# Performance work log

Measured on AMD Instinct MI355X. Metric: run time of the kernel, lower is better.

## Reference

```python
import jax, jax.numpy as jnp
import numpy as np

D_MODEL = 64  # per-head dim; temper = sqrt(D_MODEL)
NEG_INF = -1e30  # stand-in for -inf; safe under softmax and autodiff


def setup_inputs() -> dict:
    key = jax.random.key(0)
    kq, kk, kv, km = jax.random.split(key, 4)
    B, S, D = 16, 2048, 64
    q = jax.random.normal(kq, (B, S, D), dtype=jnp.float32)
    k = jax.random.normal(kk, (B, S, D), dtype=jnp.float32)
    v = jax.random.normal(kv, (B, S, D), dtype=jnp.float32)
    attn_mask = jax.random.bernoulli(km, 0.1, (B, S, S))
    return {"q": q, "k": k, "v": v, "attn_mask": attn_mask}


def reference(q, k, v, attn_mask):
    temper = jnp.sqrt(jnp.float32(D_MODEL))
    # [B, Sq, Sk] scores
    attn = jnp.einsum("bqd,bkd->bqk", q, k) / temper
    attn = jnp.where(attn_mask, NEG_INF, attn)
    attn = jax.nn.softmax(attn, axis=2)
    # dropout is identity in eval / attn_dropout=0.0
    output = jnp.einsum("bqk,bkd->bqd", attn, v)
    return (output, attn)
```

## Files before the change

kernel.cpp:

```cpp
#include <hip/hip_runtime.h>
#include <hip/hip_bf16.h>
#include <stdint.h>


#define S_DIM 2048
#define D_DIM 64

typedef short short8 __attribute__((ext_vector_type(8)));
typedef float floatx4 __attribute__((ext_vector_type(4)));
typedef unsigned short ushort8v __attribute__((ext_vector_type(8)));
typedef uint32_t u32a __attribute__((may_alias));

__device__ __forceinline__ unsigned short f2bf(float x) {
    uint32_t u = __float_as_uint(x);
    u += 0x7fffu + ((u >> 16) & 1u);
    return (unsigned short)(u >> 16);
}
__device__ __forceinline__ float bf2f(unsigned short h) {
    return __uint_as_float((uint32_t)h << 16);
}

__global__ __launch_bounds__(256) void prep_all(
    const int* __restrict__ mask, uint32_t* __restrict__ bits,
    const float* __restrict__ k,
    unsigned short* __restrict__ khi2, unsigned short* __restrict__ klo2,
    const float* __restrict__ v, unsigned short* __restrict__ vfrag)
{
    const int blk = blockIdx.x;
    const int tid = threadIdx.x;

    if (blk < 8192) {
        const size_t base = (size_t)blk * 8192;
        const int lane = tid & 63;
        const size_t wbase = base + (size_t)(tid & ~63);
        #pragma unroll
        for (int j = 0; j < 32; ++j) {
            int m = mask[base + j * 256 + tid];
            unsigned long long bal = __ballot(m != 0);
            if ((lane & 31) == 0) {
                size_t wb = wbase + j * 256;
                bits[(wb >> 5) + (lane >> 5)] = (uint32_t)(bal >> ((lane >> 5) * 32));
            }
        }
    } else if (blk < 9216) {
        const int e  = blk - 8192;
        const int b  = e >> 6;
        const int kc = (e & 63) * 2 + (tid >> 7);
        const int t  = tid & 127;
        const int s = t >> 6, quad = (t >> 4) & 3, n16 = t & 15;
        const float* src = k + ((size_t)(b * S_DIM) + kc * 16 + n16) * D_DIM + s * 32 + quad * 8;
        float4 x0 = *(const float4*)src;
        float4 x1 = *(const float4*)(src + 4);
        float xs[8] = {x0.x, x0.y, x0.z, x0.w, x1.x, x1.y, x1.z, x1.w};
        ushort8v h, l;
        #pragma unroll
        for (int p = 0; p < 8; ++p) {
            unsigned short hp = f2bf(xs[p]);
            h[p] = hp;
            l[p] = f2bf(xs[p] - bf2f(hp));
        }
        size_t o = ((size_t)(b * 128 + kc)) * 1024 + (size_t)t * 8;
        *(ushort8v*)(khi2 + o) = h;
        *(ushort8v*)(klo2 + o) = l;
    } else {
        const int e  = blk - 9216;
        const int b  = e >> 6;
        const int kb = e & 63;
        const int nc = tid >> 6, quad = (tid >> 4) & 3, n16 = tid & 15;
        ushort8v o;
        #pragma unroll
        for (int p = 0; p < 8; ++p) {
            float x = v[((size_t)(b * S_DIM) + kb * 32 + quad * 8 + p) * D_DIM + nc * 16 + n16];
            o[p] = f2bf(x);
        }
        *(ushort8v*)(vfrag + ((size_t)(b * 64 + kb)) * 2048 + (size_t)tid * 8) = o;
    }
}

__global__ __launch_bounds__(512) void attn_fused_v4(
    const float* __restrict__ q,
    const unsigned short* __restrict__ khi2, const unsigned short* __restrict__ klo2,
    const unsigned short* __restrict__ vfrag,
    const uint32_t* __restrict__ bits,
    float* __restrict__ out, float* __restrict__ attn)
{
    __shared__ __align__(16) float qlds[16 * 68];
    __shared__ __align__(16) unsigned short pbuf[8 * 16 * 36];
    __shared__ __align__(16) float obuf[8 * 16 * 68];
    __shared__ float mxtab[8 * 16];
    __shared__ float ltab[8 * 16];

    const int tid  = threadIdx.x;
    const int w    = tid >> 6;
    const int lane = tid & 63;
    const int quad = lane >> 4;
    const int n16  = lane & 15;
    const int b    = blockIdx.x >> 7;
    const int q0   = (blockIdx.x & 127) * 16;
    const int key0 = w * 256;

    uint32_t blo, bhi;
    {
        const uint32_t* bsrc = bits +
            ((size_t)(b * S_DIM) + q0 + (lane >> 2)) * 64 + w * 8 + 2 * (lane & 3);
        uint2 bt = *(const uint2*)bsrc;
        blo = bt.x; bhi = bt.y;
    }

    {
        int m = tid >> 5, d = (tid & 31) * 2;
        float2 qv = *(const float2*)(q + ((size_t)(b * S_DIM + q0 + m)) * D_DIM + d);
        qlds[m * 68 + d]     = qv.x;
        qlds[m * 68 + d + 1] = qv.y;
    }
    __syncthreads();

    short8 ahi[2], alo[2];
    #pragma unroll
    for (int s = 0; s < 2; ++s) {
        const float* qp = &qlds[n16 * 68 + s * 32 + quad * 8];
        union { unsigned short u[8]; short8 v; } H, L;
        #pragma unroll
        for (int p = 0; p < 8; ++p) {
            float x = qp[p];
            unsigned short hp = f2bf(x);
            H.u[p] = hp;
            L.u[p] = f2bf(x - bf2f(hp));
        }
        ahi[s] = H.v; alo[s] = L.v;
    }

    floatx4 sc[16];
    const unsigned short* khb = khi2 + (size_t)b * 131072;
    const unsigned short* klb = klo2 + (size_t)b * 131072;
    #pragma unroll
    for (int c = 0; c < 16; ++c) {
        const int kc = w * 16 + c;
        floatx4 acc = {0.f, 0.f, 0.f, 0.f};
        #pragma unroll
        for (int s = 0; s < 2; ++s) {
            const size_t off = (size_t)((kc * 2 + s) * 4 + quad) * 128 + n16 * 8;
            short8 BH = *(const short8*)(khb + off);
            short8 BL = *(const short8*)(klb + off);
            acc = __builtin_amdgcn_mfma_f32_16x16x32_bf16(ahi[s], BH, acc, 0, 0, 0);
            acc = __builtin_amdgcn_mfma_f32_16x16x32_bf16(ahi[s], BL, acc, 0, 0, 0);
            acc = __builtin_amdgcn_mfma_f32_16x16x32_bf16(alo[s], BH, acc, 0, 0, 0);
        }
        sc[c] = acc;
    }
    #pragma unroll
    for (int r = 0; r < 4; ++r) {
        #pragma unroll
        for (int c = 0; c < 16; ++c) {
            int srcl = quad * 16 + r * 4 + (c >> 2);
            uint32_t d = (uint32_t)__shfl((int)((c & 2) ? bhi : blo), srcl, 64);
            uint32_t bit = (d >> ((c & 1) * 16 + n16)) & 1u;
            sc[c][r] = bit ? -1e30f : sc[c][r] * 0.125f;
        }
    }

    #pragma unroll
    for (int r = 0; r < 4; ++r) {
        float mx = sc[0][r];
        #pragma unroll
        for (int c = 1; c < 16; ++c) mx = fmaxf(mx, sc[c][r]);
        #pragma unroll
        for (int o = 1; o < 16; o <<= 1) mx = fmaxf(mx, __shfl_xor(mx, o, 64));
        if (n16 == 0) mxtab[w * 16 + quad * 4 + r] = mx;
    }
    __syncthreads();
    #pragma unroll
    for (int r = 0; r < 4; ++r) {
        float mf = -3e38f;
        #pragma unroll
        for (int w2 = 0; w2 < 8; ++w2) mf = fmaxf(mf, mxtab[w2 * 16 + quad * 4 + r]);
        float l = 0.f;
        #pragma unroll
        for (int c = 0; c < 16; ++c) {
            float e = __expf(sc[c][r] - mf);
            sc[c][r] = e;
            l += e;
        }
        #pragma unroll
        for (int o = 1; o < 16; o <<= 1) l += __shfl_xor(l, o, 64);
        if (n16 == 0) ltab[w * 16 + quad * 4 + r] = l;
    }
    __syncthreads();
    #pragma unroll
    for (int r = 0; r < 4; ++r) {
        float l = 0.f;
        #pragma unroll
        for (int w2 = 0; w2 < 8; ++w2) l += ltab[w2 * 16 + quad * 4 + r];
        float inv = 1.0f / l;
        #pragma unroll
        for (int c = 0; c < 16; ++c) sc[c][r] *= inv;
    }

    {
        float* arow = attn + (size_t)(b * S_DIM + q0 + quad * 4) * S_DIM + key0 + n16;
        #pragma unroll
        for (int c = 0; c < 16; ++c) {
            #pragma unroll
            for (int r = 0; r < 4; ++r)
                __builtin_nontemporal_store(sc[c][r], arow + (size_t)r * S_DIM + c * 16);
        }
    }

    floatx4 o0 = {0,0,0,0}, o1 = {0,0,0,0}, o2 = {0,0,0,0}, o3 = {0,0,0,0};
    unsigned short* pw = pbuf + w * 576;
    const unsigned short* vtb = vfrag + (size_t)b * 131072;
    #pragma unroll
    for (int s2 = 0; s2 < 8; ++s2) {
        #pragma unroll
        for (int h = 0; h < 2; ++h) {
            const int c = s2 * 2 + h;
            #pragma unroll
            for (int r = 0; r < 4; ++r)
                pw[(quad * 4 + r) * 36 + h * 16 + n16] = f2bf(sc[c][r]);
        }
        short8 pa;
        {
            const u32a* pr = (const u32a*)((const char*)pbuf +
                                   (size_t)w * 1152 + n16 * 72 + quad * 16);
            union { uint32_t u[4]; short8 v; } P;
            P.u[0] = pr[0]; P.u[1] = pr[1]; P.u[2] = pr[2]; P.u[3] = pr[3];
            pa = P.v;
        }
        const int kb = w * 8 + s2;
        #pragma unroll
        for (int nc = 0; nc < 4; ++nc) {
            const size_t off = (size_t)((kb * 4 + nc) * 4 + quad) * 128 + n16 * 8;
            short8 bv = *(const short8*)(vtb + off);
            floatx4& oo = (nc == 0 ? o0 : nc == 1 ? o1 : nc == 2 ? o2 : o3);
            oo = __builtin_amdgcn_mfma_f32_16x16x32_bf16(pa, bv, oo, 0, 0, 0);
        }
    }

    #pragma unroll
    for (int nc = 0; nc < 4; ++nc) {
        floatx4 oo = (nc == 0 ? o0 : nc == 1 ? o1 : nc == 2 ? o2 : o3);
        #pragma unroll
        for (int i = 0; i < 4; ++i)
            obuf[(w * 16 + quad * 4 + i) * 68 + nc * 16 + n16] = oo[i];
    }
    __syncthreads();
    #pragma unroll
    for (int t2 = 0; t2 < 2; ++t2) {
        int idx = tid + t2 * 512;
        int m = idx >> 6, d = idx & 63;
        float a = 0.f;
        #pragma unroll
        for (int w2 = 0; w2 < 8; ++w2) a += obuf[(w2 * 16 + m) * 68 + d];
        out[(size_t)(b * S_DIM + q0 + m) * D_DIM + d] = a;
    }
}

__global__ __launch_bounds__(512) void attn_fused_v1(
    const float* __restrict__ q, const float* __restrict__ k,
    const float* __restrict__ v, const int* __restrict__ mask,
    float* __restrict__ out, float* __restrict__ attn)
{
    __shared__ __align__(16) float qlds[16 * 68];
    __shared__ __align__(16) unsigned short pbuf[8 * 16 * 36];
    __shared__ __align__(16) float obuf[8 * 16 * 68];
    __shared__ float mxtab[8 * 16];
    __shared__ float ltab[8 * 16];

    const int tid  = threadIdx.x;
    const int w    = tid >> 6;
    const int lane = tid & 63;
    const int quad = lane >> 4;
    const int n16  = lane & 15;
    const int b    = blockIdx.x >> 7;
    const int q0   = (blockIdx.x & 127) * 16;
    const int key0 = w * 256;

    {
        int m = tid >> 5, d = (tid & 31) * 2;
        float2 qv = *(const float2*)(q + ((size_t)(b * S_DIM + q0 + m)) * D_DIM + d);
        qlds[m * 68 + d]     = qv.x;
        qlds[m * 68 + d + 1] = qv.y;
    }
    __syncthreads();

    short8 ahi[2], alo[2];
    #pragma unroll
    for (int s = 0; s < 2; ++s) {
        const float* qp = &qlds[n16 * 68 + s * 32 + quad * 8];
        union { __hip_bfloat162 h[4]; short8 v; } H, L;
        #pragma unroll
        for (int p = 0; p < 4; ++p) {
            float x0 = qp[2 * p], x1 = qp[2 * p + 1];
            __hip_bfloat162 h2 = __float22bfloat162_rn(float2{x0, x1});
            float l0 = x0 - __bfloat162float(h2.x);
            float l1 = x1 - __bfloat162float(h2.y);
            H.h[p] = h2;
            L.h[p] = __float22bfloat162_rn(float2{l0, l1});
        }
        ahi[s] = H.v; alo[s] = L.v;
    }

    floatx4 sc[16];
    const size_t kvbase = (size_t)(b * S_DIM) * D_DIM;
    #pragma unroll
    for (int c = 0; c < 16; ++c) {
        const int key = key0 + c * 16 + n16;
        const int* mp = mask + (size_t)(b * S_DIM + q0 + quad * 4) * S_DIM + key;
        int mk0 = mp[0], mk1 = mp[S_DIM], mk2 = mp[2 * S_DIM], mk3 = mp[3 * S_DIM];
        floatx4 acc = {0.f, 0.f, 0.f, 0.f};
        #pragma unroll
        for (int s = 0; s < 2; ++s) {
            const float* kp = k + kvbase + (size_t)key * D_DIM + s * 32 + quad * 8;
            float4 k0 = *(const float4*)kp;
            float4 k1 = *(const float4*)(kp + 4);
            float kf[8] = {k0.x, k0.y, k0.z, k0.w, k1.x, k1.y, k1.z, k1.w};
            union { __hip_bfloat162 h[4]; short8 v; } BH, BL;
            #pragma unroll
            for (int p = 0; p < 4; ++p) {
                float x0 = kf[2 * p], x1 = kf[2 * p + 1];
                __hip_bfloat162 h2 = __float22bfloat162_rn(float2{x0, x1});
                BH.h[p] = h2;
                BL.h[p] = __float22bfloat162_rn(
                    float2{x0 - __bfloat162float(h2.x), x1 - __bfloat162float(h2.y)});
            }
            acc = __builtin_amdgcn_mfma_f32_16x16x32_bf16(ahi[s], BH.v, acc, 0, 0, 0);
            acc = __builtin_amdgcn_mfma_f32_16x16x32_bf16(ahi[s], BL.v, acc, 0, 0, 0);
            acc = __builtin_amdgcn_mfma_f32_16x16x32_bf16(alo[s], BH.v, acc, 0, 0, 0);
        }
        sc[c][0] = mk0 ? -1e30f : acc[0] * 0.125f;
        sc[c][1] = mk1 ? -1e30f : acc[1] * 0.125f;
        sc[c][2] = mk2 ? -1e30f : acc[2] * 0.125f;
        sc[c][3] = mk3 ? -1e30f : acc[3] * 0.125f;
    }

    #pragma unroll
    for (int r = 0; r < 4; ++r) {
        float mx = sc[0][r];
        #pragma unroll
        for (int c = 1; c < 16; ++c) mx = fmaxf(mx, sc[c][r]);
        #pragma unroll
        for (int o = 1; o < 16; o <<= 1) mx = fmaxf(mx, __shfl_xor(mx, o, 64));
        if (n16 == 0) mxtab[w * 16 + quad * 4 + r] = mx;
    }
    __syncthreads();
    #pragma unroll
    for (int r = 0; r < 4; ++r) {
        float mf = -3e38f;
        #pragma unroll
        for (int w2 = 0; w2 < 8; ++w2) mf = fmaxf(mf, mxtab[w2 * 16 + quad * 4 + r]);
        float l = 0.f;
        #pragma unroll
        for (int c = 0; c < 16; ++c) {
            float e = __expf(sc[c][r] - mf);
            sc[c][r] = e;
            l += e;
        }
        #pragma unroll
        for (int o = 1; o < 16; o <<= 1) l += __shfl_xor(l, o, 64);
        if (n16 == 0) ltab[w * 16 + quad * 4 + r] = l;
    }
    __syncthreads();
    #pragma unroll
    for (int r = 0; r < 4; ++r) {
        float l = 0.f;
        #pragma unroll
        for (int w2 = 0; w2 < 8; ++w2) l += ltab[w2 * 16 + quad * 4 + r];
        float inv = 1.0f / l;
        #pragma unroll
        for (int c = 0; c < 16; ++c) sc[c][r] *= inv;
    }

    {
        float* arow = attn + (size_t)(b * S_DIM + q0 + quad * 4) * S_DIM + key0 + n16;
        #pragma unroll
        for (int c = 0; c < 16; ++c) {
            #pragma unroll
            for (int r = 0; r < 4; ++r) arow[(size_t)r * S_DIM + c * 16] = sc[c][r];
        }
    }

    floatx4 o0 = {0,0,0,0}, o1 = {0,0,0,0}, o2 = {0,0,0,0}, o3 = {0,0,0,0};
    unsigned short* pw = pbuf + w * 576;
    #pragma unroll
    for (int s2 = 0; s2 < 8; ++s2) {
        #pragma unroll
        for (int h = 0; h < 2; ++h) {
            const int c = s2 * 2 + h;
            #pragma unroll
            for (int r = 0; r < 4; ++r)
                pw[(quad * 4 + r) * 36 + h * 16 + n16] = f2bf(sc[c][r]);
        }
        __syncthreads();
        short8 pa;
        {
            const uint32_t* pr = (const uint32_t*)((const char*)pbuf +
                                   (size_t)w * 1152 + n16 * 72 + quad * 16);
            union { uint32_t u[4]; short8 v; } P;
            P.u[0] = pr[0]; P.u[1] = pr[1]; P.u[2] = pr[2]; P.u[3] = pr[3];
            pa = P.v;
        }
        const size_t vrow0 = (size_t)(b * S_DIM + key0 + s2 * 32 + quad * 8) * D_DIM;
        #pragma unroll
        for (int nc = 0; nc < 4; ++nc) {
            const float* vp = v + vrow0 + nc * 16 + n16;
            union { __hip_bfloat162 h[4]; short8 v8; } BV;
            #pragma unroll
            for (int p = 0; p < 4; ++p) {
                float x0 = vp[(size_t)(2 * p) * D_DIM];
                float x1 = vp[(size_t)(2 * p + 1) * D_DIM];
                BV.h[p] = __float22bfloat162_rn(float2{x0, x1});
            }
            floatx4& oo = (nc == 0 ? o0 : nc == 1 ? o1 : nc == 2 ? o2 : o3);
            oo = __builtin_amdgcn_mfma_f32_16x16x32_bf16(pa, BV.v8, oo, 0, 0, 0);
        }
        __syncthreads();
    }

    #pragma unroll
    for (int nc = 0; nc < 4; ++nc) {
        floatx4 oo = (nc == 0 ? o0 : nc == 1 ? o1 : nc == 2 ? o2 : o3);
        #pragma unroll
        for (int i = 0; i < 4; ++i)
            obuf[(w * 16 + quad * 4 + i) * 68 + nc * 16 + n16] = oo[i];
    }
    __syncthreads();
    #pragma unroll
    for (int t2 = 0; t2 < 2; ++t2) {
        int idx = tid + t2 * 512;
        int m = idx >> 6, d = idx & 63;
        float a = 0.f;
        #pragma unroll
        for (int w2 = 0; w2 < 8; ++w2) a += obuf[(w2 * 16 + m) * 68 + d];
        out[(size_t)(b * S_DIM + q0 + m) * D_DIM + d] = a;
    }
}

extern "C" void kernel_launch(void* const* d_in, const int* in_sizes, int n_in,
                              void* d_out, int out_size, void* d_ws, size_t ws_size,
                              hipStream_t stream) {
    const float* q    = (const float*)d_in[0];
    const float* k    = (const float*)d_in[1];
    const float* v    = (const float*)d_in[2];
    const int*   mask = (const int*)d_in[3];

    float* out  = (float*)d_out;
    float* attn = out + (size_t)16 * S_DIM * D_DIM;

    const size_t NE = (size_t)16 * S_DIM * D_DIM;
    const size_t need = NE * 2 * 3 + NE * 4;
    if (d_ws != nullptr && ws_size >= need) {
        unsigned short* khi2  = (unsigned short*)d_ws;
        unsigned short* klo2  = khi2 + NE;
        unsigned short* vfrag = klo2 + NE;
        uint32_t*       bits  = (uint32_t*)(vfrag + NE);
        prep_all<<<dim3(10240), dim3(256), 0, stream>>>(mask, bits, k, khi2, klo2, v, vfrag);
        attn_fused_v4<<<dim3(2048), dim3(512), 0, stream>>>(q, khi2, klo2, vfrag, bits, out, attn);
    } else {
        attn_fused_v1<<<dim3(2048), dim3(512), 0, stream>>>(q, k, v, mask, out, attn);
    }
}
```

Baseline: 580.2 us.

## Split key range across 16 waves per block with XCD-aware block swizzle

Doubles the workgroup to 1024 threads so each of 16 waves handles 128 keys instead of 256, which halves the per-thread score registers. It also adds a block-index swizzle that maps consecutive blocks onto different XCDs, and replaces the nontemporal attn stores with plain stores. The output reduction gains an extra two-phase LDS accumulation step. The intent is more parallelism and lower register pressure per thread, at the cost of more cross-wave reductions and synchronisation.

```diff
diff --git a/kernel.cpp b/kernel.cpp
--- a/kernel.cpp
+++ b/kernel.cpp
@@ -77,7 +77,7 @@
     }
 }
 
-__global__ __launch_bounds__(512) void attn_fused_v4(
+__global__ __launch_bounds__(1024) void attn_fused_v6(
     const float* __restrict__ q,
     const unsigned short* __restrict__ khi2, const unsigned short* __restrict__ klo2,
     const unsigned short* __restrict__ vfrag,
@@ -85,33 +85,27 @@
     float* __restrict__ out, float* __restrict__ attn)
 {
     __shared__ __align__(16) float qlds[16 * 68];
-    __shared__ __align__(16) unsigned short pbuf[8 * 16 * 36];
+    __shared__ __align__(16) unsigned short pbuf[16 * 16 * 36];
     __shared__ __align__(16) float obuf[8 * 16 * 68];
-    __shared__ float mxtab[8 * 16];
-    __shared__ float ltab[8 * 16];
+    __shared__ float mxtab[16 * 16];
+    __shared__ float ltab[16 * 16];
 
     const int tid  = threadIdx.x;
     const int w    = tid >> 6;
     const int lane = tid & 63;
     const int quad = lane >> 4;
     const int n16  = lane & 15;
-    const int b    = blockIdx.x >> 7;
-    const int q0   = (blockIdx.x & 127) * 16;
-    const int key0 = w * 256;
-
-    uint32_t blo, bhi;
+    const int wg   = blockIdx.x;
+    const int swz  = (wg & 7) * 256 + (wg >> 3);
+    const int b    = swz >> 7;
+    const int q0   = (swz & 127) * 16;
+    const int key0 = w * 128;
+
+    uint32_t bmask = bits[((size_t)(b * S_DIM) + q0 + (lane >> 2)) * 64 + w * 4 + (lane & 3)];
+
     {
-        const uint32_t* bsrc = bits +
-            ((size_t)(b * S_DIM) + q0 + (lane >> 2)) * 64 + w * 8 + 2 * (lane & 3);
-        uint2 bt = *(const uint2*)bsrc;
-        blo = bt.x; bhi = bt.y;
-    }
-
-    {
-        int m = tid >> 5, d = (tid & 31) * 2;
-        float2 qv = *(const float2*)(q + ((size_t)(b * S_DIM + q0 + m)) * D_DIM + d);
-        qlds[m * 68 + d]     = qv.x;
-        qlds[m * 68 + d + 1] = qv.y;
+        int m = tid >> 6, d = tid & 63;
+        qlds[m * 68 + d] = q[((size_t)(b * S_DIM + q0 + m)) * D_DIM + d];
     }
     __syncthreads();
 
@@ -130,12 +124,12 @@
         ahi[s] = H.v; alo[s] = L.v;
     }
 
-    floatx4 sc[16];
+    floatx4 sc[8];
     const unsigned short* khb = khi2 + (size_t)b * 131072;
     const unsigned short* klb = klo2 + (size_t)b * 131072;
     #pragma unroll
-    for (int c = 0; c < 16; ++c) {
-        const int kc = w * 16 + c;
+    for (int c = 0; c < 8; ++c) {
+        const int kc = w * 8 + c;
         floatx4 acc = {0.f, 0.f, 0.f, 0.f};
         #pragma unroll
         for (int s = 0; s < 2; ++s) {
@@ -151,9 +145,9 @@
     #pragma unroll
     for (int r = 0; r < 4; ++r) {
         #pragma unroll
-        for (int c = 0; c < 16; ++c) {
-            int srcl = quad * 16 + r * 4 + (c >> 2);
-            uint32_t d = (uint32_t)__shfl((int)((c & 2) ? bhi : blo), srcl, 64);
+        for (int c = 0; c < 8; ++c) {
+            int srcl = (quad * 4 + r) * 4 + (c >> 1);
+            uint32_t d = (uint32_t)__shfl((int)bmask, srcl, 64);
             uint32_t bit = (d >> ((c & 1) * 16 + n16)) & 1u;
             sc[c][r] = bit ? -1e30f : sc[c][r] * 0.125f;
         }
@@ -163,7 +157,7 @@
     for (int r = 0; r < 4; ++r) {
         float mx = sc[0][r];
         #pragma unroll
-        for (int c = 1; c < 16; ++c) mx = fmaxf(mx, sc[c][r]);
+        for (int c = 1; c < 8; ++c) mx = fmaxf(mx, sc[c][r]);
         #pragma unroll
         for (int o = 1; o < 16; o <<= 1) mx = fmaxf(mx, __shfl_xor(mx, o, 64));
         if (n16 == 0) mxtab[w * 16 + quad * 4 + r] = mx;
@@ -173,10 +167,10 @@
     for (int r = 0; r < 4; ++r) {
         float mf = -3e38f;
         #pragma unroll
-        for (int w2 = 0; w2 < 8; ++w2) mf = fmaxf(mf, mxtab[w2 * 16 + quad * 4 + r]);
+        for (int w2 = 0; w2 < 16; ++w2) mf = fmaxf(mf, mxtab[w2 * 16 + quad * 4 + r]);
         float l = 0.f;
         #pragma unroll
-        for (int c = 0; c < 16; ++c) {
+        for (int c = 0; c < 8; ++c) {
             float e = __expf(sc[c][r] - mf);
             sc[c][r] = e;
             l += e;
@@ -190,19 +184,18 @@
     for (int r = 0; r < 4; ++r) {
         float l = 0.f;
         #pragma unroll
-        for (int w2 = 0; w2 < 8; ++w2) l += ltab[w2 * 16 + quad * 4 + r];
+        for (int w2 = 0; w2 < 16; ++w2) l += ltab[w2 * 16 + quad * 4 + r];
         float inv = 1.0f / l;
         #pragma unroll
-        for (int c = 0; c < 16; ++c) sc[c][r] *= inv;
+        for (int c = 0; c < 8; ++c) sc[c][r] *= inv;
     }
 
     {
         float* arow = attn + (size_t)(b * S_DIM + q0 + quad * 4) * S_DIM + key0 + n16;
         #pragma unroll
-        for (int c = 0; c < 16; ++c) {
-            #pragma unroll
-            for (int r = 0; r < 4; ++r)
-                __builtin_nontemporal_store(sc[c][r], arow + (size_t)r * S_DIM + c * 16);
+        for (int c = 0; c < 8; ++c) {
+            #pragma unroll
+            for (int r = 0; r < 4; ++r) arow[(size_t)r * S_DIM + c * 16] = sc[c][r];
         }
     }
 
@@ -210,7 +203,7 @@
     unsigned short* pw = pbuf + w * 576;
     const unsigned short* vtb = vfrag + (size_t)b * 131072;
     #pragma unroll
-    for (int s2 = 0; s2 < 8; ++s2) {
+    for (int s2 = 0; s2 < 4; ++s2) {
         #pragma unroll
         for (int h = 0; h < 2; ++h) {
             const int c = s2 * 2 + h;
@@ -226,7 +219,7 @@
             P.u[0] = pr[0]; P.u[1] = pr[1]; P.u[2] = pr[2]; P.u[3] = pr[3];
             pa = P.v;
         }
-        const int kb = w * 8 + s2;
+        const int kb = w * 4 + s2;
         #pragma unroll
         for (int nc = 0; nc < 4; ++nc) {
             const size_t off = (size_t)((kb * 4 + nc) * 4 + quad) * 128 + n16 * 8;
@@ -236,18 +229,28 @@
         }
     }
 
-    #pragma unroll
-    for (int nc = 0; nc < 4; ++nc) {
-        floatx4 oo = (nc == 0 ? o0 : nc == 1 ? o1 : nc == 2 ? o2 : o3);
-        #pragma unroll
-        for (int i = 0; i < 4; ++i)
-            obuf[(w * 16 + quad * 4 + i) * 68 + nc * 16 + n16] = oo[i];
-    }
-    __syncthreads();
-    #pragma unroll
-    for (int t2 = 0; t2 < 2; ++t2) {
-        int idx = tid + t2 * 512;
-        int m = idx >> 6, d = idx & 63;
+    if (w < 8) {
+        #pragma unroll
+        for (int nc = 0; nc < 4; ++nc) {
+            floatx4 oo = (nc == 0 ? o0 : nc == 1 ? o1 : nc == 2 ? o2 : o3);
+            #pragma unroll
+            for (int i = 0; i < 4; ++i)
+                obuf[(w * 16 + quad * 4 + i) * 68 + nc * 16 + n16] = oo[i];
+        }
+    }
+    __syncthreads();
+    if (w >= 8) {
+        #pragma unroll
+        for (int nc = 0; nc < 4; ++nc) {
+            floatx4 oo = (nc == 0 ? o0 : nc == 1 ? o1 : nc == 2 ? o2 : o3);
+            #pragma unroll
+            for (int i = 0; i < 4; ++i)
+                obuf[((w - 8) * 16 + quad * 4 + i) * 68 + nc * 16 + n16] += oo[i];
+        }
+    }
+    __syncthreads();
+    {
+        int m = tid >> 6, d = tid & 63;
         float a = 0.f;
         #pragma unroll
         for (int w2 = 0; w2 < 8; ++w2) a += obuf[(w2 * 16 + m) * 68 + d];
@@ -454,7 +457,7 @@
         unsigned short* vfrag = klo2 + NE;
         uint32_t*       bits  = (uint32_t*)(vfrag + NE);
         prep_all<<<dim3(10240), dim3(256), 0, stream>>>(mask, bits, k, khi2, klo2, v, vfrag);
-        attn_fused_v4<<<dim3(2048), dim3(512), 0, stream>>>(q, khi2, klo2, vfrag, bits, out, attn);
+        attn_fused_v6<<<dim3(2048), dim3(1024), 0, stream>>>(q, khi2, klo2, vfrag, bits, out, attn);
     } else {
         attn_fused_v1<<<dim3(2048), dim3(512), 0, stream>>>(q, k, v, mask, out, attn);
     }
```

Result: faster. 557.7 us (-3.9%).
